# Performance work log

Hardware: AMD Instinct MI355X
Metric: run time of the kernel (lower is better)

Reference implementation:

```python
import jax, jax.numpy as jnp
import numpy as np

K = 3
STRIDE = 1
PAD = 1


def setup_inputs() -> dict:
    key = jax.random.key(0)
    k1, k2, k3 = jax.random.split(key, 3)
    N, C, H, W = 4, 256, 64, 64
    outC = 256
    x = jax.random.normal(k1, (N, C, H, W), dtype=jnp.float32)
    # offset/mask conv params (torch inits these to 0; small random makes the test nontrivial)
    conv_offset_w = jax.random.normal(k2, (3 * K * K, C, K, K), dtype=jnp.float32) * 0.01
    conv_offset_b = jnp.zeros((3 * K * K,), dtype=jnp.float32)
    # xavier-normal scale for dcn weight
    fan = C * K * K + outC * K * K
    dcn_weight = jax.random.normal(k3, (outC, C, K, K), dtype=jnp.float32) * np.float32(np.sqrt(2.0 / fan))
    return {"x": x, "conv_offset_w": conv_offset_w, "conv_offset_b": conv_offset_b, "dcn_weight": dcn_weight}


def _dcn(x, w_off, b_off, dcn_weight):
    k, s, p = K, STRIDE, PAD
    N, C, H, W = x.shape
    outC = dcn_weight.shape[0]
    KK = k * k
    # offset/mask prediction conv
    om = jax.lax.conv_general_dilated(
        x, w_off, (s, s), [(p, p), (p, p)],
        dimension_numbers=("NCHW", "OIHW", "NCHW")) + b_off[None, :, None, None]
    offset = om[:, : 2 * KK]
    mask = jax.nn.sigmoid(om[:, 2 * KK:])
    oH = (H + 2 * p - (k - 1)) // s
    oW = (W + 2 * p - (k - 1)) // s
    # pad with an extra row/col at bottom-right so floor+1 indexing is in-bounds (as in torch code)
    px = jnp.pad(x, ((0, 0), (0, 0), (p, p + 1), (p, p + 1)))
    px = jnp.transpose(px, (0, 2, 3, 1))  # (N, H+2p+1, W+2p+1, C)
    offset = jnp.transpose(offset, (0, 2, 3, 1)).reshape(N, oH, oW, KK, 2)  # (...,(y,x))
    mask = jnp.transpose(mask, (0, 2, 3, 1))  # (N, oH, oW, KK)
    base_y = jnp.arange(oH, dtype=jnp.float32) * s + p
    base_x = jnp.arange(oW, dtype=jnp.float32) * s + p
    half = (k - 1) // 2
    inner_y = jnp.repeat(jnp.arange(k, dtype=jnp.float32) - half, k)  # kernel-tap y offsets
    inner_x = jnp.tile(jnp.arange(k, dtype=jnp.float32) - half, k)   # kernel-tap x offsets
    pos_y = base_y[None, :, None, None] + inner_y[None, None, None, :] + offset[..., 0]
    pos_x = base_x[None, None, :, None] + inner_x[None, None, None, :] + offset[..., 1]
    pos_y = jnp.clip(pos_y, 0.0, H + 2 * p - 1.0)
    pos_x = jnp.clip(pos_x, 0.0, W + 2 * p - 1.0)
    y1 = jnp.floor(pos_y)
    x1 = jnp.floor(pos_x)
    y1i = y1.astype(jnp.int32)
    x1i = x1.astype(jnp.int32)
    nidx = jnp.arange(N)[:, None, None, None]
    # bilinear gathers: each (N, oH, oW, KK, C)
    v1 = px[nidx, y1i, x1i]
    v2 = px[nidx, y1i, x1i + 1]
    v3 = px[nidx, y1i + 1, x1i]
    v4 = px[nidx, y1i + 1, x1i + 1]
    lh = (pos_y - y1)[..., None]
    lw = (pos_x - x1)[..., None]
    hh = 1.0 - lh
    hw = 1.0 - lw
    value = hh * hw * v1 + hh * lw * v2 + lh * hw * v3 + lh * lw * v4
    value = value * mask[..., None]  # modulated
    w = dcn_weight.reshape(outC, C, KK)
    # sum over in_C and kernel taps -> NCHW output
    out = jnp.einsum("nhwkc,ock->nohw", value, w)
    return out


def reference(x, conv_offset_w, conv_offset_b, dcn_weight):
    return _dcn(x, conv_offset_w, conv_offset_b, dcn_weight)
```

## Files before the change

### kernel.cpp

```cpp
#include <hip/hip_runtime.h>


typedef __bf16 bf16x8 __attribute__((ext_vector_type(8)));
typedef float  f32x4  __attribute__((ext_vector_type(4)));
typedef unsigned short ushort8 __attribute__((ext_vector_type(8)));

#define XBF_OFF   0u
#define WREP_OFF  8388608u
#define WMAIN_OFF 8536064u
#define OM_OFF    9715712u

__device__ __forceinline__ unsigned short f2bf(float f) {
  unsigned int u = __float_as_uint(f);
  u += 0x7fffu + ((u >> 16) & 1u);
  return (unsigned short)(u >> 16);
}
__device__ __forceinline__ float bf2f(unsigned short h) {
  return __uint_as_float(((unsigned int)h) << 16);
}

__global__ __launch_bounds__(256) void k_transpose(const float* __restrict__ x,
                                                   unsigned short* __restrict__ xbf) {
  __shared__ float tile[32][65];
  int n  = blockIdx.z;
  int cb = blockIdx.y;
  int xb = blockIdx.x;
  int t  = threadIdx.x;
  int xx  = t & 63;
  int cc0 = t >> 6;
#pragma unroll
  for (int j = 0; j < 8; ++j) {
    int cc = cc0 + j * 4;
    tile[cc][xx] = x[((size_t)(n * 256 + cb * 32 + cc) << 12) + xb * 64 + xx];
  }
  __syncthreads();
  int ccw = t & 31;
  int xw0 = t >> 5;
#pragma unroll
  for (int j = 0; j < 8; ++j) {
    int xw = xw0 + j * 8;
    xbf[((size_t)((n << 12) + xb * 64 + xw)) * 256 + cb * 32 + ccw] = f2bf(tile[ccw][xw]);
  }
}

__global__ __launch_bounds__(256) void k_repack(const float* __restrict__ w_off,
                                                const float* __restrict__ dcn_w,
                                                unsigned short* __restrict__ wrep,
                                                unsigned short* __restrict__ wmain) {
  int idx = blockIdx.x * 256 + threadIdx.x;
  if (idx < 32 * 2304) {
    int oc  = idx / 2304;
    int rem = idx - oc * 2304;
    int kk  = rem >> 8;
    int c   = rem & 255;
    wrep[idx] = f2bf((oc < 27) ? w_off[oc * 2304 + c * 9 + kk] : 0.f);
  } else {
    int j = idx - 32 * 2304;
    int oc  = j / 2304;
    int rem = j - oc * 2304;
    int kk  = rem >> 8;
    int c   = rem & 255;
    wmain[j] = f2bf(dcn_w[oc * 2304 + c * 9 + kk]);
  }
}

__global__ __launch_bounds__(512) void k_offconv(const unsigned short* __restrict__ xbf,
                                                 const unsigned short* __restrict__ wrep,
                                                 const float* __restrict__ bias,
                                                 float* __restrict__ om) {
  __shared__ __align__(16) unsigned short SHa[2][64 * 64];
  __shared__ __align__(16) unsigned short SHb[2][32 * 64];
  int t = threadIdx.x;
  int wave = t >> 6, lane = t & 63;
  int grp = wave >> 2, wv = wave & 3;
  int tg = t & 255;
  int bm = ((blockIdx.x & 7) << 5) + (blockIdx.x >> 3);
  int n = bm >> 6, oy = bm & 63;

  unsigned short* As = SHa[grp];
  unsigned short* Bs = SHb[grp];

  int arow = tg >> 2, acc4 = tg & 3;
  int brow = tg >> 3, bch = tg & 7;

  f32x4 acc0 = {0.f, 0.f, 0.f, 0.f};
  f32x4 acc1 = {0.f, 0.f, 0.f, 0.f};

  ushort8 av[2]; ushort8 bv;
  auto prefetch = [&](int ktg) {
    int kk = ktg >> 2;
    int c0 = (ktg & 3) * 64;
    int dy = kk / 3 - 1, dx = kk % 3 - 1;
    int yy = oy + dy, xxg = arow + dx;
    bool ok = ((unsigned)yy < 64u) && ((unsigned)xxg < 64u);
    const unsigned short* p = xbf + (size_t)(((n * 64 + yy) * 64 + xxg) * 256 + c0 + acc4 * 16);
#pragma unroll
    for (int g = 0; g < 2; ++g)
      av[g] = ok ? *(const ushort8*)(p + g * 8) : (ushort8){0,0,0,0,0,0,0,0};
    bv = *(const ushort8*)(wrep + (size_t)brow * 2304 + ktg * 64 + bch * 8);
  };

  prefetch(grp * 18);
  int mr = lane & 15, q = lane >> 4;
  for (int kt = 0; kt < 18; ++kt) {
    __syncthreads();
#pragma unroll
    for (int g = 0; g < 2; ++g) {
      int ch = (acc4 * 2 + g) ^ (arow & 7);
      *(ushort8*)&As[arow * 64 + ch * 8] = av[g];
    }
    { int ch = bch ^ (brow & 7);
      *(ushort8*)&Bs[brow * 64 + ch * 8] = bv; }
    __syncthreads();
    if (kt < 17) prefetch(grp * 18 + kt + 1);
#pragma unroll
    for (int kh = 0; kh < 2; ++kh) {
      int coff = ((q + kh * 4) ^ (mr & 7)) * 8;
      bf16x8 a  = *(const bf16x8*)&As[(wv * 16 + mr) * 64 + coff];
      bf16x8 b0 = *(const bf16x8*)&Bs[mr * 64 + coff];
      bf16x8 b1 = *(const bf16x8*)&Bs[(16 + mr) * 64 + coff];
      acc0 = __builtin_amdgcn_mfma_f32_16x16x32_bf16(a, b0, acc0, 0, 0, 0);
      acc1 = __builtin_amdgcn_mfma_f32_16x16x32_bf16(a, b1, acc1, 0, 0, 0);
    }
  }
  float* scratch = (float*)&SHa[0][0];
  __syncthreads();
  if (grp == 1) {
#pragma unroll
    for (int nt = 0; nt < 2; ++nt) {
      f32x4 a = nt ? acc1 : acc0;
#pragma unroll
      for (int rg = 0; rg < 4; ++rg)
        scratch[(wv * 16 + q * 4 + rg) * 32 + nt * 16 + mr] = a[rg];
    }
  }
  __syncthreads();
  if (grp == 0) {
    int r0 = bm * 64;
#pragma unroll
    for (int nt = 0; nt < 2; ++nt) {
      f32x4 a = nt ? acc1 : acc0;
      int oc = nt * 16 + mr;
      float bvl = (oc < 27) ? bias[oc] : 0.f;
#pragma unroll
      for (int rg = 0; rg < 4; ++rg) {
        int pl = wv * 16 + q * 4 + rg;
        float v = a[rg] + scratch[pl * 32 + oc] + bvl;
        if (oc >= 18 && oc < 27) v = 1.f / (1.f + __expf(-v));
        om[(r0 + pl) * 32 + oc] = v;
      }
    }
  }
}

__global__ __launch_bounds__(1024) void k_gemm_fused(const unsigned short* __restrict__ xbf,
                                                     const float* __restrict__ om,
                                                     const unsigned short* __restrict__ wB,
                                                     float* __restrict__ out) {
  __shared__ __align__(16) unsigned short SH[4][128 * 64];
  int t = threadIdx.x;
  int wave = t >> 6, lane = t & 63;
  int grp = wave >> 3, wv = wave & 7;
  int wm = wv & 1, wn = wv >> 1;
  int tg = t & 511;
  int bmx = ((blockIdx.x & 7) << 4) + (blockIdx.x >> 3);
  int r0 = bmx * 128, o0 = blockIdx.y * 128;

  unsigned short* As = SH[grp];
  unsigned short* Bs = SH[2 + grp];

  int srow = tg >> 2, sc4 = tg & 3;
  int r = r0 + srow;
  int n = r >> 12, yx = r & 4095, oy = yx >> 6, ox = yx & 63;
  const unsigned short* xb = xbf + (size_t)n * (4096 * 256);
  const float* omr = om + (size_t)r * 32;

  const unsigned short* Bg = wB + (size_t)(o0 + srow) * 2304 + sc4 * 16;

  f32x4 acc[4][2];
#pragma unroll
  for (int mt = 0; mt < 4; ++mt)
#pragma unroll
    for (int nt = 0; nt < 2; ++nt) acc[mt][nt] = (f32x4){0.f, 0.f, 0.f, 0.f};

  float w1, w2, w3, w4;
  int a1, a2, a3, a4;
  auto params = [&](int kk) {
    float offy = omr[2 * kk], offx = omr[2 * kk + 1], m = omr[18 + kk];
    float py = (float)(oy + kk / 3) + offy;
    float px = (float)(ox + kk % 3) + offx;
    py = fminf(fmaxf(py, 0.f), 65.f);
    px = fminf(fmaxf(px, 0.f), 65.f);
    float fy = floorf(py), fx = floorf(px);
    float ly = py - fy, lx = px - fx;
    float hy = 1.f - ly, hx = 1.f - lx;
    int iy = (int)fy, ix = (int)fx;
    bool yv0 = (iy >= 1) && (iy <= 64);
    bool yv1 = (iy <= 63);
    bool xv0 = (ix >= 1) && (ix <= 64);
    bool xv1 = (ix <= 63);
    int y0 = min(max(iy - 1, 0), 63);
    int y1 = min(iy, 63);
    int x0 = min(max(ix - 1, 0), 63);
    int x1 = min(ix, 63);
    w1 = (yv0 && xv0) ? hy * hx * m : 0.f;
    w2 = (yv0 && xv1) ? hy * lx * m : 0.f;
    w3 = (yv1 && xv0) ? ly * hx * m : 0.f;
    w4 = (yv1 && xv1) ? ly * lx * m : 0.f;
    a1 = ((y0 << 6) + x0) * 256;
    a2 = ((y0 << 6) + x1) * 256;
    a3 = ((y1 << 6) + x0) * 256;
    a4 = ((y1 << 6) + x1) * 256;
  };

  ushort8 g1[2], g2[2], g3[2], g4[2], bv[2];
  auto prefetch = [&](int ktg) {
    int c0 = (ktg & 3) * 64 + sc4 * 16;
#pragma unroll
    for (int g = 0; g < 2; ++g) {
      int c = c0 + g * 8;
      g1[g] = *(const ushort8*)(xb + a1 + c);
      g2[g] = *(const ushort8*)(xb + a2 + c);
      g3[g] = *(const ushort8*)(xb + a3 + c);
      g4[g] = *(const ushort8*)(xb + a4 + c);
      bv[g] = *(const ushort8*)(Bg + ktg * 64 + g * 8);
    }
  };

  params((grp * 18) >> 2);
  prefetch(grp * 18);

  int mr = lane & 15, q = lane >> 4;
  for (int kt = 0; kt < 18; ++kt) {
    int ktg = grp * 18 + kt;
    ushort8 res[2];
#pragma unroll
    for (int g = 0; g < 2; ++g) {
#pragma unroll
      for (int j = 0; j < 8; ++j) {
        float v = w1 * bf2f(g1[g][j]) + w2 * bf2f(g2[g][j]) +
                  w3 * bf2f(g3[g][j]) + w4 * bf2f(g4[g][j]);
        res[g][j] = f2bf(v);
      }
    }
    __syncthreads();
#pragma unroll
    for (int g = 0; g < 2; ++g) {
      int ch = (sc4 * 2 + g) ^ (srow & 7);
      *(ushort8*)&As[srow * 64 + ch * 8] = res[g];
      *(ushort8*)&Bs[srow * 64 + ch * 8] = bv[g];
    }
    __syncthreads();
    if (kt < 17) {
      int nktg = ktg + 1;
      if ((nktg & 3) == 0) params(nktg >> 2);
      prefetch(nktg);
    }
#pragma unroll
    for (int kh = 0; kh < 2; ++kh) {
      int coff = ((q + kh * 4) ^ (mr & 7)) * 8;
      bf16x8 af[4], bfv[2];
#pragma unroll
      for (int mt = 0; mt < 4; ++mt)
        af[mt] = *(const bf16x8*)&As[(wm * 64 + mt * 16 + mr) * 64 + coff];
#pragma unroll
      for (int nt = 0; nt < 2; ++nt)
        bfv[nt] = *(const bf16x8*)&Bs[(wn * 32 + nt * 16 + mr) * 64 + coff];
#pragma unroll
      for (int mt = 0; mt < 4; ++mt)
#pragma unroll
        for (int nt = 0; nt < 2; ++nt)
          acc[mt][nt] = __builtin_amdgcn_mfma_f32_16x16x32_bf16(af[mt], bfv[nt], acc[mt][nt], 0, 0, 0);
    }
  }

  float* scratch = (float*)&SH[0][0];
  __syncthreads();
  if (grp == 1) {
#pragma unroll
    for (int mt = 0; mt < 4; ++mt)
#pragma unroll
      for (int nt = 0; nt < 2; ++nt) {
        int pl = wm * 64 + mt * 16 + q * 4;
        int ol = wn * 32 + nt * 16 + mr;
#pragma unroll
        for (int rg = 0; rg < 4; ++rg)
          scratch[(pl + rg) * 128 + ol] = acc[mt][nt][rg];
      }
  }
  __syncthreads();
  if (grp == 0) {
#pragma unroll
    for (int mt = 0; mt < 4; ++mt)
#pragma unroll
      for (int nt = 0; nt < 2; ++nt) {
        int pl = wm * 64 + mt * 16 + q * 4;
        int ol = wn * 32 + nt * 16 + mr;
        f32x4 v = acc[mt][nt];
#pragma unroll
        for (int rg = 0; rg < 4; ++rg) v[rg] += scratch[(pl + rg) * 128 + ol];
        int p = r0 + pl;
        int o = o0 + ol;
        int nn = p >> 12, pyx = p & 4095;
        *(f32x4*)(out + ((size_t)(nn * 256 + o) << 12) + pyx) = v;
      }
  }
}

extern "C" void kernel_launch(void* const* d_in, const int* in_sizes, int n_in,
                              void* d_out, int out_size, void* d_ws, size_t ws_size,
                              hipStream_t stream) {
  const float* x     = (const float*)d_in[0];
  const float* w_off = (const float*)d_in[1];
  const float* b_off = (const float*)d_in[2];
  const float* dcn_w = (const float*)d_in[3];
  float* out = (float*)d_out;
  char* ws = (char*)d_ws;
  unsigned short* xbf   = (unsigned short*)(ws + XBF_OFF);
  unsigned short* wrep  = (unsigned short*)(ws + WREP_OFF);
  unsigned short* wmain = (unsigned short*)(ws + WMAIN_OFF);
  float*          om    = (float*)(ws + OM_OFF);

  k_transpose<<<dim3(64, 8, 4), 256, 0, stream>>>(x, xbf);
  k_repack<<<(288 * 2304) / 256, 256, 0, stream>>>(w_off, dcn_w, wrep, wmain);
  k_offconv<<<256, 512, 0, stream>>>(xbf, wrep, b_off, om);
  k_gemm_fused<<<dim3(128, 2), 1024, 0, stream>>>(xbf, om, wmain, out);
}
```

Before: 138.4 us.

## Merge preprocessing kernels, double-buffer offconv prefetch, reorder gemm gathers around barriers

Folds the input transpose and weight repack into one launch to cut kernel launch overhead. The offset conv now prefetches two k-steps ahead into two register slots, and barriers become an LDS-only waitcnt plus s_barrier so outstanding global loads stay in flight across them. In the fused GEMM, the next step's bilinear gathers are issued before the LDS store barrier and the weight loads after it, to overlap more global latency with compute. bf16 packing switches to a cheaper perm-based rounding that drops round-to-nearest-even tie handling and adds register pressure.

```diff
diff --git a/kernel.cpp b/kernel.cpp
--- a/kernel.cpp
+++ b/kernel.cpp
@@ -4,12 +4,15 @@
 typedef __bf16 bf16x8 __attribute__((ext_vector_type(8)));
 typedef float  f32x4  __attribute__((ext_vector_type(4)));
 typedef unsigned short ushort8 __attribute__((ext_vector_type(8)));
+typedef unsigned int   uint4v  __attribute__((ext_vector_type(4)));
 
 #define XBF_OFF   0u
 #define WREP_OFF  8388608u
 #define WMAIN_OFF 8536064u
 #define OM_OFF    9715712u
 
+#define LGKM0_BAR() do { __builtin_amdgcn_s_waitcnt(0xC07F); __builtin_amdgcn_s_barrier(); } while (0)
+
 __device__ __forceinline__ unsigned short f2bf(float f) {
   unsigned int u = __float_as_uint(f);
   u += 0x7fffu + ((u >> 16) & 1u);
@@ -19,48 +22,50 @@
   return __uint_as_float(((unsigned int)h) << 16);
 }
 
-__global__ __launch_bounds__(256) void k_transpose(const float* __restrict__ x,
-                                                   unsigned short* __restrict__ xbf) {
+__global__ __launch_bounds__(256) void k_pre(const float* __restrict__ x,
+                                             const float* __restrict__ w_off,
+                                             const float* __restrict__ dcn_w,
+                                             unsigned short* __restrict__ xbf,
+                                             unsigned short* __restrict__ wrep,
+                                             unsigned short* __restrict__ wmain) {
   __shared__ float tile[32][65];
-  int n  = blockIdx.z;
-  int cb = blockIdx.y;
-  int xb = blockIdx.x;
-  int t  = threadIdx.x;
-  int xx  = t & 63;
-  int cc0 = t >> 6;
-#pragma unroll
-  for (int j = 0; j < 8; ++j) {
-    int cc = cc0 + j * 4;
-    tile[cc][xx] = x[((size_t)(n * 256 + cb * 32 + cc) << 12) + xb * 64 + xx];
-  }
-  __syncthreads();
-  int ccw = t & 31;
-  int xw0 = t >> 5;
-#pragma unroll
-  for (int j = 0; j < 8; ++j) {
-    int xw = xw0 + j * 8;
-    xbf[((size_t)((n << 12) + xb * 64 + xw)) * 256 + cb * 32 + ccw] = f2bf(tile[ccw][xw]);
-  }
-}
-
-__global__ __launch_bounds__(256) void k_repack(const float* __restrict__ w_off,
-                                                const float* __restrict__ dcn_w,
-                                                unsigned short* __restrict__ wrep,
-                                                unsigned short* __restrict__ wmain) {
-  int idx = blockIdx.x * 256 + threadIdx.x;
-  if (idx < 32 * 2304) {
-    int oc  = idx / 2304;
-    int rem = idx - oc * 2304;
-    int kk  = rem >> 8;
-    int c   = rem & 255;
-    wrep[idx] = f2bf((oc < 27) ? w_off[oc * 2304 + c * 9 + kk] : 0.f);
+  int b = blockIdx.x;
+  int t = threadIdx.x;
+  if (b < 2048) {
+    int n  = b >> 9;
+    int cb = (b >> 6) & 7;
+    int xb = b & 63;
+    int xx  = t & 63;
+    int cc0 = t >> 6;
+#pragma unroll
+    for (int j = 0; j < 8; ++j) {
+      int cc = cc0 + j * 4;
+      tile[cc][xx] = x[((size_t)(n * 256 + cb * 32 + cc) << 12) + xb * 64 + xx];
+    }
+    __syncthreads();
+    int ccw = t & 31;
+    int xw0 = t >> 5;
+#pragma unroll
+    for (int j = 0; j < 8; ++j) {
+      int xw = xw0 + j * 8;
+      xbf[((size_t)((n << 12) + xb * 64 + xw)) * 256 + cb * 32 + ccw] = f2bf(tile[ccw][xw]);
+    }
   } else {
-    int j = idx - 32 * 2304;
-    int oc  = j / 2304;
-    int rem = j - oc * 2304;
-    int kk  = rem >> 8;
-    int c   = rem & 255;
-    wmain[j] = f2bf(dcn_w[oc * 2304 + c * 9 + kk]);
+    int idx = (b - 2048) * 256 + t;
+    if (idx < 32 * 2304) {
+      int oc  = idx / 2304;
+      int rem = idx - oc * 2304;
+      int kk  = rem >> 8;
+      int c   = rem & 255;
+      wrep[idx] = f2bf((oc < 27) ? w_off[oc * 2304 + c * 9 + kk] : 0.f);
+    } else {
+      int j = idx - 32 * 2304;
+      int oc  = j / 2304;
+      int rem = j - oc * 2304;
+      int kk  = rem >> 8;
+      int c   = rem & 255;
+      wmain[j] = f2bf(dcn_w[oc * 2304 + c * 9 + kk]);
+    }
   }
 }
 
@@ -86,8 +91,8 @@
   f32x4 acc0 = {0.f, 0.f, 0.f, 0.f};
   f32x4 acc1 = {0.f, 0.f, 0.f, 0.f};
 
-  ushort8 av[2]; ushort8 bv;
-  auto prefetch = [&](int ktg) {
+  ushort8 av[2][2]; ushort8 bv[2];
+  auto prefetch = [&](int ktg, int slot) {
     int kk = ktg >> 2;
     int c0 = (ktg & 3) * 64;
     int dy = kk / 3 - 1, dx = kk % 3 - 1;
@@ -96,23 +101,26 @@
     const unsigned short* p = xbf + (size_t)(((n * 64 + yy) * 64 + xxg) * 256 + c0 + acc4 * 16);
 #pragma unroll
     for (int g = 0; g < 2; ++g)
-      av[g] = ok ? *(const ushort8*)(p + g * 8) : (ushort8){0,0,0,0,0,0,0,0};
-    bv = *(const ushort8*)(wrep + (size_t)brow * 2304 + ktg * 64 + bch * 8);
+      av[slot][g] = ok ? *(const ushort8*)(p + g * 8) : (ushort8){0,0,0,0,0,0,0,0};
+    bv[slot] = *(const ushort8*)(wrep + (size_t)brow * 2304 + ktg * 64 + bch * 8);
   };
 
-  prefetch(grp * 18);
+  int k0 = grp * 18;
+  prefetch(k0, 0);
+  prefetch(k0 + 1, 1);
   int mr = lane & 15, q = lane >> 4;
   for (int kt = 0; kt < 18; ++kt) {
-    __syncthreads();
+    int slot = kt & 1;
+    LGKM0_BAR();
 #pragma unroll
     for (int g = 0; g < 2; ++g) {
       int ch = (acc4 * 2 + g) ^ (arow & 7);
-      *(ushort8*)&As[arow * 64 + ch * 8] = av[g];
+      *(ushort8*)&As[arow * 64 + ch * 8] = av[slot][g];
     }
     { int ch = bch ^ (brow & 7);
-      *(ushort8*)&Bs[brow * 64 + ch * 8] = bv; }
-    __syncthreads();
-    if (kt < 17) prefetch(grp * 18 + kt + 1);
+      *(ushort8*)&Bs[brow * 64 + ch * 8] = bv[slot]; }
+    if (kt + 2 < 18) prefetch(k0 + kt + 2, slot);
+    LGKM0_BAR();
 #pragma unroll
     for (int kh = 0; kh < 2; ++kh) {
       int coff = ((q + kh * 4) ^ (mr & 7)) * 8;
@@ -174,7 +182,6 @@
   int n = r >> 12, yx = r & 4095, oy = yx >> 6, ox = yx & 63;
   const unsigned short* xb = xbf + (size_t)n * (4096 * 256);
   const float* omr = om + (size_t)r * 32;
-
   const unsigned short* Bg = wB + (size_t)(o0 + srow) * 2304 + sc4 * 16;
 
   f32x4 acc[4][2];
@@ -214,7 +221,7 @@
   };
 
   ushort8 g1[2], g2[2], g3[2], g4[2], bv[2];
-  auto prefetch = [&](int ktg) {
+  auto prefA = [&](int ktg) {
     int c0 = (ktg & 3) * 64 + sc4 * 16;
 #pragma unroll
     for (int g = 0; g < 2; ++g) {
@@ -223,39 +230,49 @@
       g2[g] = *(const ushort8*)(xb + a2 + c);
       g3[g] = *(const ushort8*)(xb + a3 + c);
       g4[g] = *(const ushort8*)(xb + a4 + c);
+    }
+  };
+  auto prefB = [&](int ktg) {
+#pragma unroll
+    for (int g = 0; g < 2; ++g)
       bv[g] = *(const ushort8*)(Bg + ktg * 64 + g * 8);
-    }
   };
 
-  params((grp * 18) >> 2);
-  prefetch(grp * 18);
+  int ktg0 = grp * 18;
+  params(ktg0 >> 2);
+  prefA(ktg0);
+  prefB(ktg0);
 
   int mr = lane & 15, q = lane >> 4;
   for (int kt = 0; kt < 18; ++kt) {
-    int ktg = grp * 18 + kt;
-    ushort8 res[2];
+    int ktg = ktg0 + kt;
+    uint4v rs[2];
 #pragma unroll
     for (int g = 0; g < 2; ++g) {
 #pragma unroll
-      for (int j = 0; j < 8; ++j) {
-        float v = w1 * bf2f(g1[g][j]) + w2 * bf2f(g2[g][j]) +
-                  w3 * bf2f(g3[g][j]) + w4 * bf2f(g4[g][j]);
-        res[g][j] = f2bf(v);
+      for (int p = 0; p < 4; ++p) {
+        float va = w1 * bf2f(g1[g][2 * p])     + w2 * bf2f(g2[g][2 * p]) +
+                   w3 * bf2f(g3[g][2 * p])     + w4 * bf2f(g4[g][2 * p]);
+        float vb = w1 * bf2f(g1[g][2 * p + 1]) + w2 * bf2f(g2[g][2 * p + 1]) +
+                   w3 * bf2f(g3[g][2 * p + 1]) + w4 * bf2f(g4[g][2 * p + 1]);
+        unsigned ua = __float_as_uint(va) + 0x8000u;
+        unsigned ub = __float_as_uint(vb) + 0x8000u;
+        rs[g][p] = __builtin_amdgcn_perm(ub, ua, 0x07060302u);
       }
     }
-    __syncthreads();
+    if (kt < 17) {
+      if (((ktg + 1) & 3) == 0) params((ktg + 1) >> 2);
+      prefA(ktg + 1);
+    }
+    LGKM0_BAR();
 #pragma unroll
     for (int g = 0; g < 2; ++g) {
       int ch = (sc4 * 2 + g) ^ (srow & 7);
-      *(ushort8*)&As[srow * 64 + ch * 8] = res[g];
+      *(uint4v*)&As[srow * 64 + ch * 8] = rs[g];
       *(ushort8*)&Bs[srow * 64 + ch * 8] = bv[g];
     }
-    __syncthreads();
-    if (kt < 17) {
-      int nktg = ktg + 1;
-      if ((nktg & 3) == 0) params(nktg >> 2);
-      prefetch(nktg);
-    }
+    if (kt < 17) prefB(ktg + 1);
+    LGKM0_BAR();
 #pragma unroll
     for (int kh = 0; kh < 2; ++kh) {
       int coff = ((q + kh * 4) ^ (mr & 7)) * 8;
@@ -321,8 +338,7 @@
   unsigned short* wmain = (unsigned short*)(ws + WMAIN_OFF);
   float*          om    = (float*)(ws + OM_OFF);
 
-  k_transpose<<<dim3(64, 8, 4), 256, 0, stream>>>(x, xbf);
-  k_repack<<<(288 * 2304) / 256, 256, 0, stream>>>(w_off, dcn_w, wrep, wmain);
+  k_pre<<<2048 + 2592, 256, 0, stream>>>(x, w_off, dcn_w, xbf, wrep, wmain);
   k_offconv<<<256, 512, 0, stream>>>(xbf, wrep, b_off, om);
   k_gemm_fused<<<dim3(128, 2), 1024, 0, stream>>>(xbf, om, wmain, out);
 }
```

Result: faster. 134.7 us (-2.7%).
